# Kernel optimization log

Hardware: AMD Instinct MI355X
Metric: run time of the kernel (lower is better)

## Reference

```python
import jax, jax.numpy as jnp
import numpy as np

NUM_TASKS = 8
NUM_EXPERTS = 8
TOPK = 2
WEX = 0.01
N_TOKENS = 4194304


def setup_inputs() -> dict:
    key = jax.random.key(0)
    k1, k2 = jax.random.split(key)
    router_logits = jax.random.normal(k1, (N_TOKENS, NUM_EXPERTS), dtype=jnp.float32)
    router_labels = jax.random.randint(k2, (N_TOKENS,), 0, NUM_TASKS, dtype=jnp.int64)
    return {"router_logits": router_logits, "router_labels": router_labels}


def reference(router_logits, router_labels):
    # call_update: detached softmax over experts
    probs = jax.lax.stop_gradient(
        jax.nn.softmax(router_logits.astype(jnp.float32), axis=-1)
    )  # [N, E]
    labels = router_labels.astype(jnp.int32)
    # Torch loop `for task in router_labels` adds segment_sum[task] once per
    # occurrence of task -> EX_task_gate[t] = count[t] * segment_sum[t]
    seg_sum = jax.ops.segment_sum(probs, labels, num_segments=NUM_TASKS)  # [T, E]
    counts = jax.ops.segment_sum(
        jnp.ones((probs.shape[0],), dtype=jnp.float32), labels, num_segments=NUM_TASKS
    )  # [T]
    EX_gate = seg_sum * counts[:, None]  # [T, E]
    # calculate_mutual_information_loss
    tot = EX_gate.sum() / TOPK
    EX_gate = EX_gate / (tot + 0.0001)
    P_TI = EX_gate.sum(axis=1, keepdims=True) + 0.0001  # [T, 1]
    P_EI = EX_gate.sum(axis=0, keepdims=True) + 0.0001  # [1, E]
    expert_loss = -(EX_gate * jnp.log(EX_gate / P_TI / P_EI + 0.0001)).sum()
    return jnp.float32(WEX) * expert_loss
```

## Files before the change

kernel.cpp:

```cpp
#include <hip/hip_runtime.h>
#include <hip/hip_bf16.h>

#define N_TOKENS   4194304
#define NUM_EXPERTS 8
#define NUM_TASKS   8

__global__ __launch_bounds__(256, 4) void mi_reduce_kernel(
    const float* __restrict__ logits,
    const int*   __restrict__ labels,
    float*       __restrict__ ws) {

  float acc[NUM_TASKS][NUM_EXPERTS];
  float cnt[NUM_TASKS];
#pragma unroll
  for (int t = 0; t < NUM_TASKS; ++t) {
    cnt[t] = 0.0f;
#pragma unroll
    for (int e = 0; e < NUM_EXPERTS; ++e) acc[t][e] = 0.0f;
  }

  const int stride = gridDim.x * blockDim.x;
  for (int i = blockIdx.x * blockDim.x + threadIdx.x; i < N_TOKENS; i += stride) {
    const float4* rp = reinterpret_cast<const float4*>(logits + (size_t)i * NUM_EXPERTS);
    float4 v0 = rp[0];
    float4 v1 = rp[1];
    int lab = labels[i];

    float l[8] = {v0.x, v0.y, v0.z, v0.w, v1.x, v1.y, v1.z, v1.w};
    float mx = fmaxf(fmaxf(fmaxf(l[0], l[1]), fmaxf(l[2], l[3])),
                     fmaxf(fmaxf(l[4], l[5]), fmaxf(l[6], l[7])));
    float p[8];
    float S = 0.0f;
#pragma unroll
    for (int e = 0; e < NUM_EXPERTS; ++e) {
      p[e] = __expf(l[e] - mx);
      S += p[e];
    }
    float r = __builtin_amdgcn_rcpf(S);
#pragma unroll
    for (int e = 0; e < NUM_EXPERTS; ++e) p[e] *= r;

#pragma unroll
    for (int t = 0; t < NUM_TASKS; ++t) {
      float m = (lab == t) ? 1.0f : 0.0f;
      cnt[t] += m;
#pragma unroll
      for (int e = 0; e < NUM_EXPERTS; ++e)
        acc[t][e] = fmaf(m, p[e], acc[t][e]);
    }
  }

#pragma unroll
  for (int t = 0; t < NUM_TASKS; ++t) {
#pragma unroll
    for (int e = 0; e < NUM_EXPERTS; ++e) {
      float v = acc[t][e];
#pragma unroll
      for (int m = 1; m < 64; m <<= 1) v += __shfl_xor(v, m, 64);
      acc[t][e] = v;
    }
    float c = cnt[t];
#pragma unroll
    for (int m = 1; m < 64; m <<= 1) c += __shfl_xor(c, m, 64);
    cnt[t] = c;
  }

  __shared__ float sacc[72];
  if (threadIdx.x < 72) sacc[threadIdx.x] = 0.0f;
  __syncthreads();
  if ((threadIdx.x & 63) == 0) {
#pragma unroll
    for (int t = 0; t < NUM_TASKS; ++t) {
#pragma unroll
      for (int e = 0; e < NUM_EXPERTS; ++e)
        atomicAdd(&sacc[t * NUM_EXPERTS + e], acc[t][e]);
      atomicAdd(&sacc[64 + t], cnt[t]);
    }
  }
  __syncthreads();
  if (threadIdx.x < 72) atomicAdd(&ws[threadIdx.x], sacc[threadIdx.x]);
}

__global__ void mi_finalize_kernel(const float* __restrict__ ws,
                                   float* __restrict__ out) {
  int lane = threadIdx.x;
  int t = lane >> 3;

  float seg = ws[lane];
  float c   = ws[64 + t];
  float ex  = seg * c;

  float s = ex;
#pragma unroll
  for (int m = 1; m < 64; m <<= 1) s += __shfl_xor(s, m, 64);
  float tot = s * 0.5f;
  ex = ex / (tot + 1e-4f);

  float pti = ex;
  pti += __shfl_xor(pti, 1, 64);
  pti += __shfl_xor(pti, 2, 64);
  pti += __shfl_xor(pti, 4, 64);
  pti += 1e-4f;

  float pei = ex;
  pei += __shfl_xor(pei, 8, 64);
  pei += __shfl_xor(pei, 16, 64);
  pei += __shfl_xor(pei, 32, 64);
  pei += 1e-4f;

  float term = -ex * logf(ex / pti / pei + 1e-4f);
#pragma unroll
  for (int m = 1; m < 64; m <<= 1) term += __shfl_xor(term, m, 64);

  if (lane == 0) out[0] = 0.01f * term;
}

extern "C" void kernel_launch(void* const* d_in, const int* in_sizes, int n_in,
                              void* d_out, int out_size, void* d_ws, size_t ws_size,
                              hipStream_t stream) {
  const float* logits = (const float*)d_in[0];
  const int*   labels = (const int*)d_in[1];
  float* out = (float*)d_out;
  float* ws  = (float*)d_ws;

  hipMemsetAsync(ws, 0, 72 * sizeof(float), stream);

  mi_reduce_kernel<<<1024, 256, 0, stream>>>(logits, labels, ws);
  mi_finalize_kernel<<<1, 64, 0, stream>>>(ws, out);
}
```

Baseline: 233.0 us.

## Derive task counts from softmax row sums and use fixed-trip unrolled loop

Removes the per-task count accumulators, since each softmax row sums to one and a task's count can be recovered in the finalize kernel by summing its expert sums. This drops 8 adds per token, 8 warp reductions and the extra atomics. The reduce loop also becomes a compile-time trip count with unroll 4 and the grid doubles to 2048 blocks, which exposes more memory-level parallelism. The trade-off is that counts now carry float rounding from the softmax, and register pressure may rise because the launch-bounds occupancy hint is gone.

```diff
diff --git a/kernel.cpp b/kernel.cpp
--- a/kernel.cpp
+++ b/kernel.cpp
@@ -1,26 +1,30 @@
 #include <hip/hip_runtime.h>
 #include <hip/hip_bf16.h>
 
-#define N_TOKENS   4194304
+#define N_TOKENS    4194304
 #define NUM_EXPERTS 8
 #define NUM_TASKS   8
+#define GRID        2048
+#define BLOCK       256
+#define TOK_PER_THREAD (N_TOKENS / (GRID * BLOCK))
 
-__global__ __launch_bounds__(256, 4) void mi_reduce_kernel(
+__global__ __launch_bounds__(BLOCK) void mi_reduce_kernel(
     const float* __restrict__ logits,
     const int*   __restrict__ labels,
     float*       __restrict__ ws) {
 
   float acc[NUM_TASKS][NUM_EXPERTS];
-  float cnt[NUM_TASKS];
 #pragma unroll
-  for (int t = 0; t < NUM_TASKS; ++t) {
-    cnt[t] = 0.0f;
+  for (int t = 0; t < NUM_TASKS; ++t)
 #pragma unroll
     for (int e = 0; e < NUM_EXPERTS; ++e) acc[t][e] = 0.0f;
-  }
 
-  const int stride = gridDim.x * blockDim.x;
-  for (int i = blockIdx.x * blockDim.x + threadIdx.x; i < N_TOKENS; i += stride) {
+  const int tid = blockIdx.x * BLOCK + threadIdx.x;
+  const int S   = GRID * BLOCK;
+
+#pragma unroll 4
+  for (int k = 0; k < TOK_PER_THREAD; ++k) {
+    const int i = tid + k * S;
     const float4* rp = reinterpret_cast<const float4*>(logits + (size_t)i * NUM_EXPERTS);
     float4 v0 = rp[0];
     float4 v1 = rp[1];
@@ -30,20 +34,19 @@
     float mx = fmaxf(fmaxf(fmaxf(l[0], l[1]), fmaxf(l[2], l[3])),
                      fmaxf(fmaxf(l[4], l[5]), fmaxf(l[6], l[7])));
     float p[8];
-    float S = 0.0f;
+    float Ssum = 0.0f;
 #pragma unroll
     for (int e = 0; e < NUM_EXPERTS; ++e) {
       p[e] = __expf(l[e] - mx);
-      S += p[e];
+      Ssum += p[e];
     }
-    float r = __builtin_amdgcn_rcpf(S);
+    float r = __builtin_amdgcn_rcpf(Ssum);
 #pragma unroll
     for (int e = 0; e < NUM_EXPERTS; ++e) p[e] *= r;
 
 #pragma unroll
     for (int t = 0; t < NUM_TASKS; ++t) {
       float m = (lab == t) ? 1.0f : 0.0f;
-      cnt[t] += m;
 #pragma unroll
       for (int e = 0; e < NUM_EXPERTS; ++e)
         acc[t][e] = fmaf(m, p[e], acc[t][e]);
@@ -51,7 +54,7 @@
   }
 
 #pragma unroll
-  for (int t = 0; t < NUM_TASKS; ++t) {
+  for (int t = 0; t < NUM_TASKS; ++t)
 #pragma unroll
     for (int e = 0; e < NUM_EXPERTS; ++e) {
       float v = acc[t][e];
@@ -59,36 +62,33 @@
       for (int m = 1; m < 64; m <<= 1) v += __shfl_xor(v, m, 64);
       acc[t][e] = v;
     }
-    float c = cnt[t];
-#pragma unroll
-    for (int m = 1; m < 64; m <<= 1) c += __shfl_xor(c, m, 64);
-    cnt[t] = c;
-  }
 
-  __shared__ float sacc[72];
-  if (threadIdx.x < 72) sacc[threadIdx.x] = 0.0f;
+  __shared__ float sacc[64];
+  if (threadIdx.x < 64) sacc[threadIdx.x] = 0.0f;
   __syncthreads();
   if ((threadIdx.x & 63) == 0) {
 #pragma unroll
-    for (int t = 0; t < NUM_TASKS; ++t) {
+    for (int t = 0; t < NUM_TASKS; ++t)
 #pragma unroll
       for (int e = 0; e < NUM_EXPERTS; ++e)
         atomicAdd(&sacc[t * NUM_EXPERTS + e], acc[t][e]);
-      atomicAdd(&sacc[64 + t], cnt[t]);
-    }
   }
   __syncthreads();
-  if (threadIdx.x < 72) atomicAdd(&ws[threadIdx.x], sacc[threadIdx.x]);
+  if (threadIdx.x < 64) atomicAdd(&ws[threadIdx.x], sacc[threadIdx.x]);
 }
 
 __global__ void mi_finalize_kernel(const float* __restrict__ ws,
                                    float* __restrict__ out) {
   int lane = threadIdx.x;
-  int t = lane >> 3;
 
   float seg = ws[lane];
-  float c   = ws[64 + t];
-  float ex  = seg * c;
+
+  float c = seg;
+  c += __shfl_xor(c, 1, 64);
+  c += __shfl_xor(c, 2, 64);
+  c += __shfl_xor(c, 4, 64);
+
+  float ex = seg * c;
 
   float s = ex;
 #pragma unroll
@@ -123,8 +123,8 @@
   float* out = (float*)d_out;
   float* ws  = (float*)d_ws;
 
-  hipMemsetAsync(ws, 0, 72 * sizeof(float), stream);
+  hipMemsetAsync(ws, 0, 64 * sizeof(float), stream);
 
-  mi_reduce_kernel<<<1024, 256, 0, stream>>>(logits, labels, ws);
+  mi_reduce_kernel<<<GRID, BLOCK, 0, stream>>>(logits, labels, ws);
   mi_finalize_kernel<<<1, 64, 0, stream>>>(ws, out);
 }
```

Result: no change. 232.2 us (-0.3%).
